# Kernel tuning notes

Measured on AMD Instinct MI355X. Metric: run time of the kernel, lower is better.

## Reference

```python
import jax, jax.numpy as jnp
import numpy as np

NODES = 1024
IN_F = 512
OUT_F = 256
BATCH = 32768


def setup_inputs() -> dict:
    key = jax.random.key(0)
    k1, k2, k3 = jax.random.split(key, 3)
    bound = 1.0 / np.sqrt(NODES)  # torch Linear default init range
    x = jax.random.normal(k1, (BATCH, IN_F), dtype=jnp.float32)
    W = jax.random.uniform(k2, (NODES, NODES), dtype=jnp.float32, minval=-bound, maxval=bound)
    b = jax.random.uniform(k3, (NODES,), dtype=jnp.float32, minval=-bound, maxval=bound)
    return {"x": x, "W": W, "b": b}


def reference(x, W, b):
    # state = [x, zeros]; next = W @ state + b; output = next[out_nodes]
    # out_nodes = [nodes-1-i for i in range(out_features)]  (reversed tail)
    out_idx = jnp.arange(NODES - 1, NODES - 1 - OUT_F, -1)  # [OUT_F]
    W_sel = W[out_idx, :IN_F]                               # [OUT_F, IN_F]
    b_sel = b[out_idx]                                      # [OUT_F]
    return x @ W_sel.T + b_sel                              # [BATCH, OUT_F]
```

## Files before the change

### kernel.cpp

```cpp
#include <hip/hip_runtime.h>
#include <hip/hip_bf16.h>


#define M_TOT 32768
#define K_TOT 512
#define N_TOT 256
#define W_LD  1024

#define BM 64
#define BK 64
#define NTH 512
#define KSTEPS 8

#define A_BYTES (BM * BK * 2)
#define B_BYTES (N_TOT * BK * 2)
#define LDS_BUF (A_BYTES + B_BYTES)

typedef __bf16 bf16x8 __attribute__((ext_vector_type(8)));
typedef float  f32x4  __attribute__((ext_vector_type(4)));

static __device__ __forceinline__ bf16x8 cvt8(f32x4 a, f32x4 b) {
    bf16x8 r;
    r[0] = (__bf16)a[0]; r[1] = (__bf16)a[1]; r[2] = (__bf16)a[2]; r[3] = (__bf16)a[3];
    r[4] = (__bf16)b[0]; r[5] = (__bf16)b[1]; r[6] = (__bf16)b[2]; r[7] = (__bf16)b[3];
    return r;
}

__global__ __launch_bounds__(256)
void ng_prep(const float* __restrict__ W, unsigned char* __restrict__ img)
{
    const int id = blockIdx.x * 256 + threadIdx.x;
    const int kt = id >> 11;
    const int r  = (id >> 3) & 255;
    const int c  = id & 7;
    const float* src = W + (long)(1023 - r) * W_LD + kt * 64 + c * 8;
    f32x4 a = *(const f32x4*)src;
    f32x4 b = *(const f32x4*)(src + 4);
    *(bf16x8*)(img + kt * B_BYTES + r * 128 + ((c * 16) ^ ((r & 7) << 4))) = cvt8(a, b);
}

#define GLL16(gp_, lp_) __builtin_amdgcn_global_load_lds(                     \
        (const __attribute__((address_space(1))) void*)(gp_),                 \
        (__attribute__((address_space(3))) void*)(lp_), 16, 0, 0)

__global__ __launch_bounds__(NTH, 4)
void ng_gemm(const float* __restrict__ x, const unsigned char* __restrict__ wimg,
             const float* __restrict__ bias, float* __restrict__ out)
{
    __shared__ __align__(16) unsigned char lds[2 * LDS_BUF];

    const int tid  = threadIdx.x;
    const int lane = tid & 63;
    const int wid  = tid >> 6;
    const int wrow = wid >> 2;
    const int wcol = wid & 3;
    const long mBase = (long)blockIdx.x * BM;

    const int arow = tid >> 3;
    const int skg  = tid & 7;
    const float* srcA = x + (mBase + arow) * K_TOT + skg * 8;
    const int swzA = arow * 128 + ((skg * 16) ^ ((arow & 7) << 4));

    int rdA[2][2], rdB[2][4];
#pragma unroll
    for (int ks = 0; ks < 2; ++ks) {
        const int col = ks * 64 + (lane >> 4) * 16;
#pragma unroll
        for (int i = 0; i < 2; ++i) {
            const int ra = wrow * 32 + i * 16 + (lane & 15);
            rdA[ks][i] = ra * 128 + (col ^ ((ra & 7) << 4));
        }
#pragma unroll
        for (int j = 0; j < 4; ++j) {
            const int rb = wcol * 64 + j * 16 + (lane & 15);
            rdB[ks][j] = A_BYTES + rb * 128 + (col ^ ((rb & 7) << 4));
        }
    }

    f32x4 acc[2][4];
#pragma unroll
    for (int mi = 0; mi < 2; ++mi)
#pragma unroll
        for (int ni = 0; ni < 4; ++ni)
            acc[mi][ni] = (f32x4){0.f, 0.f, 0.f, 0.f};

    f32x4 rgA0, rgA1;

#define STAGEB(kt_, base_) do {                                               \
        const unsigned char* s_ = wimg + (kt_) * B_BYTES;                     \
        _Pragma("unroll")                                                     \
        for (int c_ = 0; c_ < 4; ++c_)                                        \
            GLL16(s_ + c_ * 8192 + tid * 16,                                  \
                  lds + (base_) + A_BYTES + c_ * 8192 + wid * 1024);          \
    } while (0)

#define LOADA(kt_) do {                                                       \
        const float* p_ = srcA + (kt_) * BK;                                  \
        rgA0 = *(const f32x4*)(p_);                                           \
        rgA1 = *(const f32x4*)(p_ + 4);                                       \
    } while (0)

#define WRITEA(base_) do {                                                    \
        *(bf16x8*)(lds + (base_) + swzA) = cvt8(rgA0, rgA1);                  \
    } while (0)

#define COMPUTET(base_) do {                                                  \
        _Pragma("unroll")                                                     \
        for (int ks_ = 0; ks_ < 2; ++ks_) {                                   \
            bf16x8 af_[2], bf_[4];                                            \
            _Pragma("unroll")                                                 \
            for (int i_ = 0; i_ < 2; ++i_)                                    \
                af_[i_] = *(const bf16x8*)(lds + (base_) + rdA[ks_][i_]);     \
            _Pragma("unroll")                                                 \
            for (int j_ = 0; j_ < 4; ++j_)                                    \
                bf_[j_] = *(const bf16x8*)(lds + (base_) + rdB[ks_][j_]);     \
            _Pragma("unroll")                                                 \
            for (int mi_ = 0; mi_ < 2; ++mi_)                                 \
                _Pragma("unroll")                                             \
                for (int ni_ = 0; ni_ < 4; ++ni_)                             \
                    acc[mi_][ni_] = __builtin_amdgcn_mfma_f32_16x16x32_bf16(  \
                        af_[mi_], bf_[ni_], acc[mi_][ni_], 0, 0, 0);          \
        }                                                                     \
    } while (0)

    STAGEB(0, 0);
    LOADA(0);
    WRITEA(0);
    __syncthreads();

#pragma unroll
    for (int t = 0; t < KSTEPS; ++t) {
        const int cur = (t & 1) * LDS_BUF;
        const int nxt = LDS_BUF - cur;
        if (t + 1 < KSTEPS) {
            STAGEB(t + 1, nxt);
            LOADA(t + 1);
        }
        COMPUTET(cur);
        if (t + 1 < KSTEPS) WRITEA(nxt);
        __syncthreads();
    }

    const int cRow = wrow * 32 + (lane >> 4) * 4;
    const int cCol = wcol * 64 + (lane & 15);
#pragma unroll
    for (int ni = 0; ni < 4; ++ni) {
        const int gn = cCol + ni * 16;
        const float bv = bias[1023 - gn];
#pragma unroll
        for (int mi = 0; mi < 2; ++mi) {
            float* dst = out + (mBase + cRow + mi * 16) * (long)N_TOT + gn;
#pragma unroll
            for (int i = 0; i < 4; ++i)
                dst[(long)i * N_TOT] = acc[mi][ni][i] + bv;
        }
    }
#undef STAGEB
#undef LOADA
#undef WRITEA
#undef COMPUTET
}

extern "C" void kernel_launch(void* const* d_in, const int* in_sizes, int n_in,
                              void* d_out, int out_size, void* d_ws, size_t ws_size,
                              hipStream_t stream) {
    const float* x = (const float*)d_in[0];
    const float* W = (const float*)d_in[1];
    const float* b = (const float*)d_in[2];
    float* out = (float*)d_out;
    unsigned char* img = (unsigned char*)d_ws;

    ng_prep<<<dim3(64), dim3(256), 0, stream>>>(W, img);
    ng_gemm<<<dim3(M_TOT / BM), dim3(NTH), 0, stream>>>(x, img, b, out);
}
```

Baseline: 113.4 us.

## Drop LDS staging and load GEMM operands directly into registers

```diff
diff --git a/kernel.cpp b/kernel.cpp
--- a/kernel.cpp
+++ b/kernel.cpp
@@ -7,14 +7,8 @@
 #define N_TOT 256
 #define W_LD  1024
 
-#define BM 64
-#define BK 64
-#define NTH 512
-#define KSTEPS 8
-
-#define A_BYTES (BM * BK * 2)
-#define B_BYTES (N_TOT * BK * 2)
-#define LDS_BUF (A_BYTES + B_BYTES)
+#define NTH 256
+#define ROWS_PER_BLK 32
 
 typedef __bf16 bf16x8 __attribute__((ext_vector_type(8)));
 typedef float  f32x4  __attribute__((ext_vector_type(4)));
@@ -27,55 +21,34 @@
 }
 
 __global__ __launch_bounds__(256)
-void ng_prep(const float* __restrict__ W, unsigned char* __restrict__ img)
+void ng_prep(const float* __restrict__ W, __bf16* __restrict__ Bm)
 {
     const int id = blockIdx.x * 256 + threadIdx.x;
-    const int kt = id >> 11;
-    const int r  = (id >> 3) & 255;
-    const int c  = id & 7;
-    const float* src = W + (long)(1023 - r) * W_LD + kt * 64 + c * 8;
+    const int n  = id >> 6;
+    const int kg = id & 63;
+    const float* src = W + (long)(1023 - n) * W_LD + kg * 8;
     f32x4 a = *(const f32x4*)src;
     f32x4 b = *(const f32x4*)(src + 4);
-    *(bf16x8*)(img + kt * B_BYTES + r * 128 + ((c * 16) ^ ((r & 7) << 4))) = cvt8(a, b);
+    *(bf16x8*)(Bm + n * K_TOT + kg * 8) = cvt8(a, b);
 }
 
-#define GLL16(gp_, lp_) __builtin_amdgcn_global_load_lds(                     \
-        (const __attribute__((address_space(1))) void*)(gp_),                 \
-        (__attribute__((address_space(3))) void*)(lp_), 16, 0, 0)
-
 __global__ __launch_bounds__(NTH, 4)
-void ng_gemm(const float* __restrict__ x, const unsigned char* __restrict__ wimg,
+void ng_gemm(const float* __restrict__ x, const __bf16* __restrict__ Bm,
              const float* __restrict__ bias, float* __restrict__ out)
 {
-    __shared__ __align__(16) unsigned char lds[2 * LDS_BUF];
+    const int lane = threadIdx.x & 63;
+    const int wcol = threadIdx.x >> 6;
+    const long mBase = (long)blockIdx.x * ROWS_PER_BLK;
 
-    const int tid  = threadIdx.x;
-    const int lane = tid & 63;
-    const int wid  = tid >> 6;
-    const int wrow = wid >> 2;
-    const int wcol = wid & 3;
-    const long mBase = (long)blockIdx.x * BM;
+    const int r16 = lane & 15;
+    const int ko  = lane >> 4;
 
-    const int arow = tid >> 3;
-    const int skg  = tid & 7;
-    const float* srcA = x + (mBase + arow) * K_TOT + skg * 8;
-    const int swzA = arow * 128 + ((skg * 16) ^ ((arow & 7) << 4));
-
-    int rdA[2][2], rdB[2][4];
-#pragma unroll
-    for (int ks = 0; ks < 2; ++ks) {
-        const int col = ks * 64 + (lane >> 4) * 16;
-#pragma unroll
-        for (int i = 0; i < 2; ++i) {
-            const int ra = wrow * 32 + i * 16 + (lane & 15);
-            rdA[ks][i] = ra * 128 + (col ^ ((ra & 7) << 4));
-        }
-#pragma unroll
-        for (int j = 0; j < 4; ++j) {
-            const int rb = wcol * 64 + j * 16 + (lane & 15);
-            rdB[ks][j] = A_BYTES + rb * 128 + (col ^ ((rb & 7) << 4));
-        }
-    }
+    const float* pa0 = x + (mBase + r16) * K_TOT + ko * 8;
+    const float* pa1 = pa0 + 16 * K_TOT;
+    const __bf16* pb0 = Bm + (wcol * 64 + r16) * K_TOT + ko * 8;
+    const __bf16* pb1 = pb0 + 16 * K_TOT;
+    const __bf16* pb2 = pb0 + 32 * K_TOT;
+    const __bf16* pb3 = pb0 + 48 * K_TOT;
 
     f32x4 acc[2][4];
 #pragma unroll
@@ -84,64 +57,42 @@
         for (int ni = 0; ni < 4; ++ni)
             acc[mi][ni] = (f32x4){0.f, 0.f, 0.f, 0.f};
 
-    f32x4 rgA0, rgA1;
+    f32x4  aE[2][2], aO[2][2];
+    bf16x8 bE[4], bO[4];
 
-#define STAGEB(kt_, base_) do {                                               \
-        const unsigned char* s_ = wimg + (kt_) * B_BYTES;                     \
-        _Pragma("unroll")                                                     \
-        for (int c_ = 0; c_ < 4; ++c_)                                        \
-            GLL16(s_ + c_ * 8192 + tid * 16,                                  \
-                  lds + (base_) + A_BYTES + c_ * 8192 + wid * 1024);          \
+#define LDSET(AA_, BB_, kk_) do {                                   \
+        AA_[0][0] = *(const f32x4*)(pa0 + (kk_) * 32);              \
+        AA_[0][1] = *(const f32x4*)(pa0 + (kk_) * 32 + 4);          \
+        AA_[1][0] = *(const f32x4*)(pa1 + (kk_) * 32);              \
+        AA_[1][1] = *(const f32x4*)(pa1 + (kk_) * 32 + 4);          \
+        BB_[0] = *(const bf16x8*)(pb0 + (kk_) * 32);                \
+        BB_[1] = *(const bf16x8*)(pb1 + (kk_) * 32);                \
+        BB_[2] = *(const bf16x8*)(pb2 + (kk_) * 32);                \
+        BB_[3] = *(const bf16x8*)(pb3 + (kk_) * 32);                \
     } while (0)
 
-#define LOADA(kt_) do {                                                       \
-        const float* p_ = srcA + (kt_) * BK;                                  \
-        rgA0 = *(const f32x4*)(p_);                                           \
-        rgA1 = *(const f32x4*)(p_ + 4);                                       \
+#define MMA(AA_, BB_) do {                                                        \
+        bf16x8 a0_ = cvt8(AA_[0][0], AA_[0][1]);                                  \
+        bf16x8 a1_ = cvt8(AA_[1][0], AA_[1][1]);                                  \
+        _Pragma("unroll")                                                         \
+        for (int ni_ = 0; ni_ < 4; ++ni_) {                                       \
+            acc[0][ni_] = __builtin_amdgcn_mfma_f32_16x16x32_bf16(                \
+                a0_, BB_[ni_], acc[0][ni_], 0, 0, 0);                             \
+            acc[1][ni_] = __builtin_amdgcn_mfma_f32_16x16x32_bf16(                \
+                a1_, BB_[ni_], acc[1][ni_], 0, 0, 0);                             \
+        }                                                                         \
     } while (0)
 
-#define WRITEA(base_) do {                                                    \
-        *(bf16x8*)(lds + (base_) + swzA) = cvt8(rgA0, rgA1);                  \
-    } while (0)
-
-#define COMPUTET(base_) do {                                                  \
-        _Pragma("unroll")                                                     \
-        for (int ks_ = 0; ks_ < 2; ++ks_) {                                   \
-            bf16x8 af_[2], bf_[4];                                            \
-            _Pragma("unroll")                                                 \
-            for (int i_ = 0; i_ < 2; ++i_)                                    \
-                af_[i_] = *(const bf16x8*)(lds + (base_) + rdA[ks_][i_]);     \
-            _Pragma("unroll")                                                 \
-            for (int j_ = 0; j_ < 4; ++j_)                                    \
-                bf_[j_] = *(const bf16x8*)(lds + (base_) + rdB[ks_][j_]);     \
-            _Pragma("unroll")                                                 \
-            for (int mi_ = 0; mi_ < 2; ++mi_)                                 \
-                _Pragma("unroll")                                             \
-                for (int ni_ = 0; ni_ < 4; ++ni_)                             \
-                    acc[mi_][ni_] = __builtin_amdgcn_mfma_f32_16x16x32_bf16(  \
-                        af_[mi_], bf_[ni_], acc[mi_][ni_], 0, 0, 0);          \
-        }                                                                     \
-    } while (0)
-
-    STAGEB(0, 0);
-    LOADA(0);
-    WRITEA(0);
-    __syncthreads();
-
+    LDSET(aE, bE, 0);
 #pragma unroll
-    for (int t = 0; t < KSTEPS; ++t) {
-        const int cur = (t & 1) * LDS_BUF;
-        const int nxt = LDS_BUF - cur;
-        if (t + 1 < KSTEPS) {
-            STAGEB(t + 1, nxt);
-            LOADA(t + 1);
-        }
-        COMPUTET(cur);
-        if (t + 1 < KSTEPS) WRITEA(nxt);
-        __syncthreads();
+    for (int kk = 0; kk < 16; kk += 2) {
+        if (kk + 1 < 16) LDSET(aO, bO, kk + 1);
+        MMA(aE, bE);
+        if (kk + 2 < 16) LDSET(aE, bE, kk + 2);
+        MMA(aO, bO);
     }
 
-    const int cRow = wrow * 32 + (lane >> 4) * 4;
+    const int cRow = (lane >> 4) * 4;
     const int cCol = wcol * 64 + (lane & 15);
 #pragma unroll
     for (int ni = 0; ni < 4; ++ni) {
@@ -155,10 +106,8 @@
                 dst[(long)i * N_TOT] = acc[mi][ni][i] + bv;
         }
     }
-#undef STAGEB
-#undef LOADA
-#undef WRITEA
-#undef COMPUTET
+#undef LDSET
+#undef MMA
 }
 
 extern "C" void kernel_launch(void* const* d_in, const int* in_sizes, int n_in,
@@ -168,8 +117,8 @@
     const float* W = (const float*)d_in[1];
     const float* b = (const float*)d_in[2];
     float* out = (float*)d_out;
-    unsigned char* img = (unsigned char*)d_ws;
+    __bf16* Bm = (__bf16*)d_ws;
 
-    ng_prep<<<dim3(64), dim3(256), 0, stream>>>(W, img);
-    ng_gemm<<<dim3(M_TOT / BM), dim3(NTH), 0, stream>>>(x, img, b, out);
+    ng_prep<<<dim3(64), dim3(256), 0, stream>>>(W, Bm);
+    ng_gemm<<<dim3(M_TOT / ROWS_PER_BLK), dim3(NTH), 0, stream>>>(x, Bm, b, out);
 }
```

After: 150.8 us. 1.33x slower.
